# Optimization experiments

Measured on AMD Instinct MI355X. Metric: run time of the kernel, lower is better.

Reference implementation:

```python
import jax, jax.numpy as jnp
import numpy as np

TAU = 2.0      # LIF membrane time constant
VTH = 1.0      # spike threshold
ALPHA = 2.0    # surrogate-gradient sharpness (atan surrogate)
EPS = 1e-5     # BatchNorm eps

@jax.custom_vjp
def spike(u):
    return (u > 0.0).astype(u.dtype)

def _spike_fwd(u):
    return spike(u), u

def _spike_bwd(u, g):
    sg = ALPHA / (2.0 * (1.0 + (jnp.pi / 2.0 * ALPHA * u) ** 2))
    return (g * sg,)

spike.defvjp(_spike_fwd, _spike_bwd)

def lif_time(x):
    # x: [B,T,C,H,W] -> spikes [B,T,C,H,W]; hard-reset LIF, v0 = 0
    xT = jnp.moveaxis(x, 1, 0)  # [T,B,C,H,W]
    def step(v, xt):
        v = v + (xt - v) / TAU
        s = spike(v - VTH)
        return v * (1.0 - s), s
    _, sT = jax.lax.scan(step, jnp.zeros_like(xT[0]), xT)
    return jnp.moveaxis(sT, 0, 1)

def conv2d(x, w, stride, pad):
    return jax.lax.conv_general_dilated(
        x, w, (stride, stride), [(pad, pad), (pad, pad)],
        dimension_numbers=('NCHW', 'OIHW', 'NCHW'))

def bn(x, gamma, beta, mean, var):
    # inference-style BatchNorm2d with running stats; x: [N,C,H,W]
    inv = gamma * jax.lax.rsqrt(var + EPS)
    return x * inv[None, :, None, None] + (beta - mean * inv)[None, :, None, None]

def setup_inputs() -> dict:
    key = jax.random.key(0)
    ks = jax.random.split(key, 16)
    B, T, Cin, Cout, H, W = 16, 8, 128, 256, 56, 56
    d = {}
    d['x_spike'] = (jax.random.uniform(ks[0], (B, T, Cin, H, W)) < 0.2).astype(jnp.float32)
    d['conv1_w'] = jax.random.normal(ks[1], (Cout, Cin, 3, 3), dtype=jnp.float32) * 0.05
    d['conv2_w'] = jax.random.normal(ks[2], (Cout, Cout, 3, 3), dtype=jnp.float32) * 0.05
    d['ds_w'] = jax.random.normal(ks[3], (Cout, Cin, 1, 1), dtype=jnp.float32) * 0.05
    for i, p in enumerate(['n1', 'n2', 'nd']):
        d[p + '_gamma'] = 1.0 + 0.1 * jax.random.normal(ks[4 + i], (Cout,), dtype=jnp.float32)
        d[p + '_beta'] = 0.1 * jax.random.normal(ks[7 + i], (Cout,), dtype=jnp.float32)
        d[p + '_mean'] = 0.01 * jax.random.normal(ks[10 + i], (Cout,), dtype=jnp.float32)
        d[p + '_var'] = jax.random.uniform(ks[13 + i], (Cout,), minval=0.5, maxval=1.5)
    return d

def reference(x_spike, conv1_w, conv2_w, ds_w,
              n1_gamma, n1_beta, n1_mean, n1_var,
              n2_gamma, n2_beta, n2_mean, n2_var,
              nd_gamma, nd_beta, nd_mean, nd_var):
    B, T, Cin, H, W = x_spike.shape
    x_flat = x_spike.reshape(B * T, Cin, H, W)
    # downsample shortcut (1x1 conv stride 2 + BN)
    identity = bn(conv2d(x_flat, ds_w, 2, 0), nd_gamma, nd_beta, nd_mean, nd_var)
    # NOTE: original module runs lif_shortcut on identity but DISCARDS the result
    # (pure state side-effect); it does not affect the output, so it is omitted.
    out = bn(conv2d(x_flat, conv1_w, 2, 1), n1_gamma, n1_beta, n1_mean, n1_var)
    Cout, Ho, Wo = out.shape[1], out.shape[2], out.shape[3]
    out = lif_time(out.reshape(B, T, Cout, Ho, Wo))
    out = bn(conv2d(out.reshape(B * T, Cout, Ho, Wo), conv2_w, 1, 1),
             n2_gamma, n2_beta, n2_mean, n2_var) + identity
    return lif_time(out.reshape(B, T, Cout, Ho, Wo))
```

## Files before the change

### kernel.cpp

```cpp
#include <hip/hip_runtime.h>

#define CIN  128
#define CO   256
#define HIN  56
#define WIN  56
#define P    784
#define HWIN 3136
#define PERT 200704

typedef __attribute__((ext_vector_type(4))) float f32x4;
typedef __attribute__((ext_vector_type(4))) int   i32x4;

__device__ __forceinline__ i32x4 mfma_i8_64(i32x4 a, i32x4 b, i32x4 c) {
    return __builtin_amdgcn_mfma_i32_16x16x64_i8(a, b, c, 0, 0, 0);
}

__device__ __forceinline__ void gld_lds16(const void* g, void* l) {
    __builtin_amdgcn_global_load_lds(
        (const __attribute__((address_space(1))) void*)g,
        (__attribute__((address_space(3))) void*)l, 16, 0, 0);
}

__global__ __launch_bounds__(256) void k_prepA(
    const float* __restrict__ g1, const float* __restrict__ b1,
    const float* __restrict__ m1, const float* __restrict__ v1,
    const float* __restrict__ g2, const float* __restrict__ b2,
    const float* __restrict__ m2, const float* __restrict__ v2,
    const float* __restrict__ gd, const float* __restrict__ bd,
    const float* __restrict__ md, const float* __restrict__ vd,
    const float* __restrict__ w1, const float* __restrict__ w2,
    const float* __restrict__ wd,
    float* __restrict__ bias1, float* __restrict__ bias2,
    float* __restrict__ qscale1, float* __restrict__ scale1,
    float* __restrict__ qscale2, float* __restrict__ scale2)
{
    const int bid = blockIdx.x;
    if (bid == 0) {
        int co = threadIdx.x;
        float inv1 = g1[co] / sqrtf(v1[co] + 1e-5f);
        float inv2 = g2[co] / sqrtf(v2[co] + 1e-5f);
        float invd = gd[co] / sqrtf(vd[co] + 1e-5f);
        bias1[co] = fmaf(-m1[co], inv1, b1[co]);
        bias2[co] = fmaf(-m2[co], inv2, b2[co]) + fmaf(-md[co], invd, bd[co]);
        return;
    }
    const int lane = threadIdx.x & 63;
    if (bid <= 64) {
        int co = (bid - 1) * 4 + (threadIdx.x >> 6);
        float iv = g1[co] / sqrtf(v1[co] + 1e-5f);
        float m = 0.f;
        for (int k = lane; k < 1152; k += 64)
            m = fmaxf(m, fabsf(w1[(size_t)co * 1152 + k] * iv));
#pragma unroll
        for (int off = 32; off > 0; off >>= 1)
            m = fmaxf(m, __shfl_xor(m, off));
        if (lane == 0) {
            int s = (int)floorf(log2f(8355000.0f / m));
            if (s > 44) s = 44;
            qscale1[co] = ldexpf(1.0f, s);
            scale1[co]  = ldexpf(1.0f, -s);
        }
    } else {
        int co = (bid - 65) * 4 + (threadIdx.x >> 6);
        float iv2 = g2[co] / sqrtf(v2[co] + 1e-5f);
        float ivd = gd[co] / sqrtf(vd[co] + 1e-5f);
        float m = 0.f;
        for (int k = lane; k < 2304; k += 64)
            m = fmaxf(m, fabsf(w2[(size_t)co * 2304 + k] * iv2));
        for (int k = lane; k < 128; k += 64)
            m = fmaxf(m, fabsf(wd[(size_t)co * 128 + k] * ivd));
#pragma unroll
        for (int off = 32; off > 0; off >>= 1)
            m = fmaxf(m, __shfl_xor(m, off));
        if (lane == 0) {
            int s = (int)floorf(log2f(8355000.0f / m));
            if (s > 40) s = 40;
            qscale2[co] = ldexpf(1.0f, s);
            scale2[co]  = ldexpf(1.0f, -s);
        }
    }
}

__global__ __launch_bounds__(256) void k_prepB(
    const float* __restrict__ w1, const float* __restrict__ w2,
    const float* __restrict__ wd,
    const float* __restrict__ n1g, const float* __restrict__ n1v,
    const float* __restrict__ n2g, const float* __restrict__ n2v,
    const float* __restrict__ ndg, const float* __restrict__ ndv,
    const float* __restrict__ qscale1, const float* __restrict__ qscale2,
    signed char* __restrict__ pa, signed char* __restrict__ pb,
    signed char* __restrict__ pc,
    signed char* __restrict__ p2a, signed char* __restrict__ p2b,
    signed char* __restrict__ p2c,
    signed char* __restrict__ pda, signed char* __restrict__ pdb,
    signed char* __restrict__ pdc,
    const float* __restrict__ x, unsigned int* __restrict__ xt_p)
{
    const int bid = blockIdx.x;
    if (bid < 72) {
        int i = bid * 256 + threadIdx.x;
        if (i >= 18432) return;
        int tap = i >> 11;
        int r   = i & 2047;
        int kg  = r >> 10;
        int r2  = r & 1023;
        int cf  = r2 >> 6;
        int lane = r2 & 63;
        int co  = cf * 16 + (lane & 15);
        int ci0 = kg * 64 + (lane >> 4) * 16;
        float iv = n1g[co] / sqrtf(n1v[co] + 1e-5f);
        float q  = qscale1[co];
#pragma unroll
        for (int j = 0; j < 16; j++) {
            float w = w1[((size_t)co * CIN + ci0 + j) * 9 + tap] * iv;
            int W = __float2int_rn(w * q);
            int d0 = ((W & 0xFF) ^ 0x80) - 0x80;  W = (W - d0) / 256;
            int d1 = ((W & 0xFF) ^ 0x80) - 0x80;  W = (W - d1) / 256;
            size_t idx = (size_t)i * 16 + j;
            pa[idx] = (signed char)W;
            pb[idx] = (signed char)d1;
            pc[idx] = (signed char)d0;
        }
    } else if (bid < 216) {
        int i = (bid - 72) * 256 + threadIdx.x;
        int tap = i >> 12;
        int r   = i & 4095;
        int kg  = r >> 10;
        int r2  = r & 1023;
        int cf  = r2 >> 6;
        int lane = r2 & 63;
        int co  = cf * 16 + (lane & 15);
        int ci0 = kg * 64 + (lane >> 4) * 16;
        float iv = n2g[co] / sqrtf(n2v[co] + 1e-5f);
        float q  = qscale2[co];
#pragma unroll
        for (int j = 0; j < 16; j++) {
            float w = w2[((size_t)co * CO + ci0 + j) * 9 + tap] * iv;
            int W = __float2int_rn(w * q);
            int d0 = ((W & 0xFF) ^ 0x80) - 0x80;  W = (W - d0) / 256;
            int d1 = ((W & 0xFF) ^ 0x80) - 0x80;  W = (W - d1) / 256;
            size_t idx = (size_t)i * 16 + j;
            p2a[idx] = (signed char)W;
            p2b[idx] = (signed char)d1;
            p2c[idx] = (signed char)d0;
        }
    } else if (bid < 224) {
        int i = (bid - 216) * 256 + threadIdx.x;
        int kg  = i >> 10;
        int r2  = i & 1023;
        int cf  = r2 >> 6;
        int lane = r2 & 63;
        int co  = cf * 16 + (lane & 15);
        int ci0 = kg * 64 + (lane >> 4) * 16;
        float iv = ndg[co] / sqrtf(ndv[co] + 1e-5f);
        float q  = qscale2[co];
#pragma unroll
        for (int j = 0; j < 16; j++) {
            float w = wd[(size_t)co * CIN + ci0 + j] * iv;
            int W = __float2int_rn(w * q);
            int d0 = ((W & 0xFF) ^ 0x80) - 0x80;  W = (W - d0) / 256;
            int d1 = ((W & 0xFF) ^ 0x80) - 0x80;  W = (W - d1) / 256;
            size_t idx = (size_t)i * 16 + j;
            pda[idx] = (signed char)W;
            pdb[idx] = (signed char)d1;
            pdc[idx] = (signed char)d0;
        }
    } else {
        int i = (bid - 224) * 256 + threadIdx.x;
        int pos = i % HWIN;
        int nw  = i / HWIN;
        int w   = nw & 3;
        int n   = nw >> 2;
        const float* xp = x + ((size_t)n * CIN + w * 32) * HWIN + pos;
        unsigned int word = 0;
#pragma unroll
        for (int ci = 0; ci < 32; ci++)
            if (xp[(size_t)ci * HWIN] != 0.f) word |= (1u << ci);
        xt_p[((size_t)n * HWIN + pos) * 4 + w] = word;
    }
}

__global__ __launch_bounds__(256) void k_conv1_mfma(
    const unsigned int* __restrict__ xt_p,
    const signed char* __restrict__ pa,
    const signed char* __restrict__ pb,
    const signed char* __restrict__ pc,
    const float* __restrict__ scale1,
    const float* __restrict__ bias1,
    float* __restrict__ out)
{
    __shared__ unsigned int XWP[2][522 * 2];

    const int n    = blockIdx.x / 7;
    const int rt   = blockIdx.x - n * 7;
    const int r0   = rt * 4;
    const int tid  = threadIdx.x;
    const int wave = tid >> 6;
    const int lane = tid & 63;
    const int l15  = lane & 15;
    const int quad = lane >> 4;
    const int cf   = blockIdx.y * 4 + wave;

    const unsigned int* xp_n = xt_p + (size_t)n * HWIN * 4;
    for (int i = tid; i < 513; i += 256) {
        int row = i / 57, c = i - row * 57;
        int irow = 2 * r0 - 1 + row;
        int iw   = c - 1;
        uint4 val = {0u, 0u, 0u, 0u};
        if (irow >= 0 && iw >= 0)
            val = *(const uint4*)(xp_n + (size_t)(irow * WIN + iw) * 4);
        int base = row * 58 + c;
        XWP[0][base * 2 + 0] = val.x;
        XWP[0][base * 2 + 1] = val.y;
        XWP[1][base * 2 + 0] = val.z;
        XWP[1][base * 2 + 1] = val.w;
    }
    __syncthreads();

    int ib[7];
#pragma unroll
    for (int f = 0; f < 7; f++) {
        int pos = f * 16 + l15;
        int rr = pos / 28, cc = pos - rr * 28;
        ib[f] = (2 * rr) * 58 + 2 * cc;
    }

    const int  qh = quad >> 1;
    const int  ql = (quad & 1) * 16;

    i32x4 accA[7], accB[7], accC[7];
#pragma unroll
    for (int f = 0; f < 7; f++) {
        accA[f] = (i32x4){0, 0, 0, 0};
        accB[f] = (i32x4){0, 0, 0, 0};
        accC[f] = (i32x4){0, 0, 0, 0};
    }

    i32x4 wa, wb, wc, na, nb, nc;
    {
        size_t b0 = (size_t)cf * 1024 + lane * 16;
        wa = *(const i32x4*)(pa + b0);
        wb = *(const i32x4*)(pb + b0);
        wc = *(const i32x4*)(pc + b0);
        na = wa; nb = wb; nc = wc;
    }

    for (int kg = 0; kg < 2; kg++) {
        for (int tap = 0; tap < 9; tap++) {
            int rd = kg * 9 + tap;
            if (rd < 17) {
                int rn = rd + 1, kn = rn / 9, tn = rn - kn * 9;
                size_t b0 = ((size_t)(tn * 2 + kn) * 16 + cf) * 1024 + lane * 16;
                na = *(const i32x4*)(pa + b0);
                nb = *(const i32x4*)(pb + b0);
                nc = *(const i32x4*)(pc + b0);
            }
            const int kh = tap / 3, kw = tap - kh * 3;
            const int tapoff = kh * 58 + kw;
#pragma unroll
            for (int f = 0; f < 7; f++) {
                int base = ib[f] + tapoff;
                uint2 pr = *(const uint2*)&XWP[kg][base * 2];
                unsigned int w32  = qh ? pr.y : pr.x;
                unsigned int bits = (w32 >> ql) & 0xFFFFu;
                uint4 u;
                u.x = ((bits & 15u)         * 0x00204081u) & 0x01010101u;
                u.y = (((bits >> 4) & 15u)  * 0x00204081u) & 0x01010101u;
                u.z = (((bits >> 8) & 15u)  * 0x00204081u) & 0x01010101u;
                u.w = ((bits >> 12)         * 0x00204081u) & 0x01010101u;
                union { uint4 q; i32x4 v; } cv;
                cv.q = u;
                __builtin_amdgcn_s_setprio(1);
                accA[f] = mfma_i8_64(wa, cv.v, accA[f]);
                accB[f] = mfma_i8_64(wb, cv.v, accB[f]);
                accC[f] = mfma_i8_64(wc, cv.v, accC[f]);
                __builtin_amdgcn_s_setprio(0);
            }
            wa = na; wb = nb; wc = nc;
        }
    }

#pragma unroll
    for (int f = 0; f < 7; f++) {
        int pg = rt * 112 + f * 16 + l15;
#pragma unroll
        for (int reg = 0; reg < 4; reg++) {
            int co = cf * 16 + quad * 4 + reg;
            float hi = (float)accA[f][reg];
            float mi = (float)accB[f][reg];
            float lo = (float)accC[f][reg];
            float val = fmaf(hi, 65536.f, fmaf(mi, 256.f, lo));
            out[((size_t)n * CO + co) * P + pg] = fmaf(val, scale1[co], bias1[co]);
        }
    }
}

__global__ __launch_bounds__(256) void k_lif1t(
    const float* __restrict__ pre, unsigned char* __restrict__ st)
{
    __shared__ unsigned short T[16 * 68];
    const int b   = blockIdx.x;
    const int co0 = blockIdx.y * 64;
    const int kg  = blockIdx.y;
    const int p0  = blockIdx.z * 16;
    const int tid  = threadIdx.x;
    const int pcol = tid & 15;
    const int g    = tid >> 4;
    const int pos = p0 + g;
    const int oh  = pos / 28, ow = pos - oh * 28;
    const int f8  = ((((oh + 1) * 30 + ow + 1) >> 1) & 3);
    const int no  = (pcol >> 2) ^ f8;
    const int wb  = (pcol & 3) * 4;
    float v[4] = {0.f, 0.f, 0.f, 0.f};
    for (int t = 0; t < 8; t++) {
        const float* src = pre + (((size_t)(b * 8 + t)) * CO + co0) * P + p0;
        unsigned short s[4];
#pragma unroll
        for (int j = 0; j < 4; j++) {
            int co = g + 16 * j;
            float xv = src[(size_t)co * P + pcol];
            v[j] = v[j] + (xv - v[j]) * 0.5f;
            bool sp = v[j] > 1.0f;
            s[j] = sp ? 1 : 0;
            if (sp) v[j] = 0.f;
        }
        __syncthreads();
#pragma unroll
        for (int j = 0; j < 4; j++) T[pcol * 68 + g + 16 * j] = s[j];
        __syncthreads();
        unsigned char* dst = st + (((size_t)(b * 8 + t) * 4 + kg) * P + pos) * 64
                               + no * 16 + wb;
        uchar4 ov;
        ov.x = (unsigned char)T[g * 68 + pcol * 4 + 0];
        ov.y = (unsigned char)T[g * 68 + pcol * 4 + 1];
        ov.z = (unsigned char)T[g * 68 + pcol * 4 + 2];
        ov.w = (unsigned char)T[g * 68 + pcol * 4 + 3];
        *(uchar4*)dst = ov;
    }
}

__global__ __launch_bounds__(256) void k_conv2_mfma(
    const unsigned char* __restrict__ spike_t,
    const unsigned int* __restrict__ xt_p,
    const signed char* __restrict__ p2a,
    const signed char* __restrict__ p2b,
    const signed char* __restrict__ p2c,
    const signed char* __restrict__ pda,
    const signed char* __restrict__ pdb,
    const signed char* __restrict__ pdc,
    const float* __restrict__ scale2,
    const float* __restrict__ bias2,
    float* __restrict__ out)
{
    __shared__ unsigned char SB[4 * 11520];
    __shared__ unsigned int  XW2[4 * 112];

    const int n    = blockIdx.x / 7;
    const int rt   = blockIdx.x - n * 7;
    const int r0   = rt * 4;
    const int tid  = threadIdx.x;
    const int wave = tid >> 6;
    const int lane = tid & 63;
    const int l15  = lane & 15;
    const int quad = lane >> 4;
    const int cf0  = blockIdx.y * 8 + wave * 2;

    {
        uint4 z = {0u, 0u, 0u, 0u};
        for (int i = tid; i < 2880; i += 256) ((uint4*)SB)[i] = z;
    }
    for (int i = tid; i < 112; i += 256) {
        int r = i / 28, c = i - r * 28;
        uint4 w4 = *(const uint4*)(xt_p + ((size_t)n * HWIN
                    + (2 * (r0 + r)) * WIN + 2 * c) * 4);
        XW2[0 * 112 + i] = w4.x;
        XW2[1 * 112 + i] = w4.y;
        XW2[2 * 112 + i] = w4.z;
        XW2[3 * 112 + i] = w4.w;
    }
    __syncthreads();

    i32x4 dw[2][3][2];
#pragma unroll
    for (int kg = 0; kg < 2; kg++) {
        size_t b0 = ((size_t)kg * 16 + cf0) * 1024 + (size_t)lane * 16;
#pragma unroll
        for (int g = 0; g < 2; g++) {
            dw[kg][0][g] = *(const i32x4*)(pda + b0 + (size_t)g * 1024);
            dw[kg][1][g] = *(const i32x4*)(pdb + b0 + (size_t)g * 1024);
            dw[kg][2][g] = *(const i32x4*)(pdc + b0 + (size_t)g * 1024);
        }
    }

    const char* sp_n = (const char*)spike_t + (size_t)n * 4 * P * 64;
#pragma unroll
    for (int k = 0; k < 3; k++) {
        int idx  = wave * 3 + k;
        int row  = idx >> 1, half = idx & 1;
        int irow = r0 - 1 + row;
        bool ok  = ((unsigned)irow < 28u) && (half == 0 || lane < 48);
        int ldso = row * 1920 + 64 + half * 1024;
        if (ok) {
#pragma unroll
            for (int kg = 0; kg < 4; kg++)
                gld_lds16(sp_n + (size_t)kg * 50176 + (size_t)irow * 1792
                              + half * 1024 + lane * 16,
                          (char*)SB + kg * 11520 + ldso);
        }
    }

    int ib[7];
#pragma unroll
    for (int f = 0; f < 7; f++) {
        int pos = f * 16 + l15;
        int rr = pos / 28, cc = pos - rr * 28;
        ib[f] = rr * 30 + cc;
    }

    i32x4 acc[3][2][7];
#pragma unroll
    for (int p = 0; p < 3; p++)
#pragma unroll
        for (int g = 0; g < 2; g++)
#pragma unroll
            for (int f = 0; f < 7; f++) acc[p][g][f] = (i32x4){0, 0, 0, 0};

#pragma unroll
    for (int kg = 0; kg < 2; kg++) {
        const int wsel = (kg * 2 + (quad >> 1)) * 112;
        const int shv  = (quad & 1) * 16;
#pragma unroll
        for (int f = 0; f < 7; f++) {
            unsigned int w32  = XW2[wsel + f * 16 + l15];
            unsigned int bits = (w32 >> shv) & 0xFFFFu;
            uint4 u;
            u.x = ((bits & 15u)         * 0x00204081u) & 0x01010101u;
            u.y = (((bits >> 4) & 15u)  * 0x00204081u) & 0x01010101u;
            u.z = (((bits >> 8) & 15u)  * 0x00204081u) & 0x01010101u;
            u.w = ((bits >> 12)         * 0x00204081u) & 0x01010101u;
            union { uint4 q; i32x4 v; } cv;
            cv.q = u;
            __builtin_amdgcn_s_setprio(1);
#pragma unroll
            for (int g = 0; g < 2; g++) {
                acc[0][g][f] = mfma_i8_64(dw[kg][0][g], cv.v, acc[0][g][f]);
                acc[1][g][f] = mfma_i8_64(dw[kg][1][g], cv.v, acc[1][g][f]);
                acc[2][g][f] = mfma_i8_64(dw[kg][2][g], cv.v, acc[2][g][f]);
            }
            __builtin_amdgcn_s_setprio(0);
        }
    }
    __syncthreads();

    i32x4 cw[2][3], nx[2][3];
#pragma unroll
    for (int g = 0; g < 2; g++) {
        size_t b0 = ((size_t)(cf0 + g)) * 1024 + (size_t)lane * 16;
        cw[g][0] = *(const i32x4*)(p2a + b0);
        cw[g][1] = *(const i32x4*)(p2b + b0);
        cw[g][2] = *(const i32x4*)(p2c + b0);
        nx[g][0] = cw[g][0]; nx[g][1] = cw[g][1]; nx[g][2] = cw[g][2];
    }

    for (int rd = 0; rd < 36; rd++) {
        if (rd < 35) {
            size_t b0 = ((size_t)(rd + 1) * 16 + cf0) * 1024
                      + (size_t)lane * 16;
#pragma unroll
            for (int g = 0; g < 2; g++) {
                nx[g][0] = *(const i32x4*)(p2a + b0 + (size_t)g * 1024);
                nx[g][1] = *(const i32x4*)(p2b + b0 + (size_t)g * 1024);
                nx[g][2] = *(const i32x4*)(p2c + b0 + (size_t)g * 1024);
            }
        }
        const int tap = rd >> 2, kg = rd & 3;
        const int kh = tap / 3, kw = tap - kh * 3;
        const int tapoff = kh * 30 + kw;
        const int sbase  = kg * 11520;
#pragma unroll
        for (int f = 0; f < 7; f++) {
            int slot = ib[f] + tapoff;
            int sw   = (slot >> 1) & 3;
            i32x4 bfr = *(const i32x4*)(
                SB + sbase + slot * 64 + ((quad ^ sw) * 16));
            __builtin_amdgcn_s_setprio(1);
#pragma unroll
            for (int g = 0; g < 2; g++) {
                acc[0][g][f] = mfma_i8_64(cw[g][0], bfr, acc[0][g][f]);
                acc[1][g][f] = mfma_i8_64(cw[g][1], bfr, acc[1][g][f]);
                acc[2][g][f] = mfma_i8_64(cw[g][2], bfr, acc[2][g][f]);
            }
            __builtin_amdgcn_s_setprio(0);
        }
#pragma unroll
        for (int g = 0; g < 2; g++) {
            cw[g][0] = nx[g][0]; cw[g][1] = nx[g][1]; cw[g][2] = nx[g][2];
        }
    }

#pragma unroll
    for (int g = 0; g < 2; g++)
#pragma unroll
        for (int f = 0; f < 7; f++) {
            int pg = rt * 112 + f * 16 + l15;
#pragma unroll
            for (int reg = 0; reg < 4; reg++) {
                int co = (cf0 + g) * 16 + quad * 4 + reg;
                float A  = (float)acc[0][g][f][reg];
                float Bv = (float)acc[1][g][f][reg];
                float Cv = (float)acc[2][g][f][reg];
                float val = fmaf(A, 65536.f, fmaf(Bv, 256.f, Cv));
                out[((size_t)n * CO + co) * P + pg] = fmaf(val, scale2[co], bias2[co]);
            }
        }
}

__global__ __launch_bounds__(256) void k_lif4(const float4* __restrict__ in,
                                              float4* __restrict__ out)
{
    const int q = PERT / 4;
    const int i = blockIdx.x * 256 + threadIdx.x;
    const int b = i / q;
    const int r = i - b * q;
    const float4* pi = in  + (size_t)(b * 8) * q + r;
    float4*       po = out + (size_t)(b * 8) * q + r;
    float v0 = 0.f, v1 = 0.f, v2 = 0.f, v3 = 0.f;
#pragma unroll
    for (int t = 0; t < 8; t++) {
        float4 xt = pi[(size_t)t * q];
        float4 s;
        v0 = v0 + (xt.x - v0) * 0.5f; s.x = (v0 > 1.0f) ? 1.f : 0.f; if (v0 > 1.0f) v0 = 0.f;
        v1 = v1 + (xt.y - v1) * 0.5f; s.y = (v1 > 1.0f) ? 1.f : 0.f; if (v1 > 1.0f) v1 = 0.f;
        v2 = v2 + (xt.z - v2) * 0.5f; s.z = (v2 > 1.0f) ? 1.f : 0.f; if (v2 > 1.0f) v2 = 0.f;
        v3 = v3 + (xt.w - v3) * 0.5f; s.w = (v3 > 1.0f) ? 1.f : 0.f; if (v3 > 1.0f) v3 = 0.f;
        po[(size_t)t * q] = s;
    }
}

extern "C" void kernel_launch(void* const* d_in, const int* in_sizes, int n_in,
                              void* d_out, int out_size, void* d_ws, size_t ws_size,
                              hipStream_t stream) {
    const float* x   = (const float*)d_in[0];
    const float* w1  = (const float*)d_in[1];
    const float* w2  = (const float*)d_in[2];
    const float* wd  = (const float*)d_in[3];
    const float* n1g = (const float*)d_in[4];
    const float* n1b = (const float*)d_in[5];
    const float* n1m = (const float*)d_in[6];
    const float* n1v = (const float*)d_in[7];
    const float* n2g = (const float*)d_in[8];
    const float* n2b = (const float*)d_in[9];
    const float* n2m = (const float*)d_in[10];
    const float* n2v = (const float*)d_in[11];
    const float* ndg = (const float*)d_in[12];
    const float* ndb = (const float*)d_in[13];
    const float* ndm = (const float*)d_in[14];
    const float* ndv = (const float*)d_in[15];

    float* out = (float*)d_out;

    char* w = (char*)d_ws;
    unsigned char*  spike_t = (unsigned char*)w;
    signed char*    p2a     = (signed char*)(w + 25690112);
    signed char*    p2b     = (signed char*)(w + 26279936);
    signed char*    p2c     = (signed char*)(w + 26869760);
    signed char*    pa      = (signed char*)(w + 27459584);
    signed char*    pb      = (signed char*)(w + 27754496);
    signed char*    pc      = (signed char*)(w + 28049408);
    signed char*    pda     = (signed char*)(w + 28344320);
    signed char*    pdb     = (signed char*)(w + 28377088);
    signed char*    pdc     = (signed char*)(w + 28409856);
    float*          qscale1 = (float*)(w + 28442624);
    float*          scale1f = (float*)(w + 28443648);
    float*          qscale2 = (float*)(w + 28444672);
    float*          scale2f = (float*)(w + 28445696);
    float*          bias2   = (float*)(w + 28446720);
    float*          bias1   = (float*)(w + 28447744);
    unsigned int*   xt_p    = (unsigned int*)(w + 28451840);

    k_prepA<<<129, 256, 0, stream>>>(
        n1g, n1b, n1m, n1v, n2g, n2b, n2m, n2v, ndg, ndb, ndm, ndv,
        w1, w2, wd, bias1, bias2, qscale1, scale1f, qscale2, scale2f);
    k_prepB<<<224 + (128 * 4 * HWIN) / 256, 256, 0, stream>>>(
        w1, w2, wd, n1g, n1v, n2g, n2v, ndg, ndv, qscale1, qscale2,
        pa, pb, pc, p2a, p2b, p2c, pda, pdb, pdc, x, xt_p);

    k_conv1_mfma<<<dim3(896, 4), 256, 0, stream>>>(
        xt_p, pa, pb, pc, scale1f, bias1, out);
    k_lif1t<<<dim3(16, 4, 49), 256, 0, stream>>>(out, spike_t);
    k_conv2_mfma<<<dim3(896, 2), 256, 0, stream>>>(
        spike_t, xt_p, p2a, p2b, p2c, pda, pdb, pdc, scale2f, bias2, out);
    k_lif4<<<(16 * (PERT / 4)) / 256, 256, 0, stream>>>(
        (const float4*)out, (float4*)out);
}
```

Before: 710.3 us.

## Fuse conv1 with first LIF over time; double-buffer conv2 spike tiles

Conv1 now loops over all 8 timesteps inside one block, keeping the LIF membrane state in registers and writing packed spike bytes directly. This removes the fp32 pre-activation round trip through global memory and the separate LIF kernel. Conv2 shrinks its shared spike buffer to two channel groups and streams the four groups with double-buffered async loads, which should raise occupancy. In exchange conv1 runs far fewer blocks (896 of 128 threads instead of 3584 of 256) and serializes the timesteps, so it has less parallelism and reloads weights every step.

Measured after the change: 808.7 us. 13.8% more time.

```diff
diff --git a/kernel.cpp b/kernel.cpp
--- a/kernel.cpp
+++ b/kernel.cpp
@@ -180,162 +180,151 @@
     }
 }
 
-__global__ __launch_bounds__(256) void k_conv1_mfma(
+__global__ __launch_bounds__(128) void k_conv1_lif(
     const unsigned int* __restrict__ xt_p,
     const signed char* __restrict__ pa,
     const signed char* __restrict__ pb,
     const signed char* __restrict__ pc,
     const float* __restrict__ scale1,
     const float* __restrict__ bias1,
-    float* __restrict__ out)
+    unsigned char* __restrict__ st)
 {
     __shared__ unsigned int XWP[2][522 * 2];
 
-    const int n    = blockIdx.x / 7;
-    const int rt   = blockIdx.x - n * 7;
+    const int b    = blockIdx.x / 7;
+    const int rt   = blockIdx.x - b * 7;
     const int r0   = rt * 4;
     const int tid  = threadIdx.x;
     const int wave = tid >> 6;
     const int lane = tid & 63;
     const int l15  = lane & 15;
     const int quad = lane >> 4;
-    const int cf   = blockIdx.y * 4 + wave;
-
-    const unsigned int* xp_n = xt_p + (size_t)n * HWIN * 4;
-    for (int i = tid; i < 513; i += 256) {
-        int row = i / 57, c = i - row * 57;
-        int irow = 2 * r0 - 1 + row;
-        int iw   = c - 1;
-        uint4 val = {0u, 0u, 0u, 0u};
-        if (irow >= 0 && iw >= 0)
-            val = *(const uint4*)(xp_n + (size_t)(irow * WIN + iw) * 4);
-        int base = row * 58 + c;
-        XWP[0][base * 2 + 0] = val.x;
-        XWP[0][base * 2 + 1] = val.y;
-        XWP[1][base * 2 + 0] = val.z;
-        XWP[1][base * 2 + 1] = val.w;
-    }
-    __syncthreads();
-
-    int ib[7];
+    const int cf   = blockIdx.y * 2 + wave;
+    const int kg_o = cf >> 2;
+    const int sub  = cf & 3;
+
+    int ib[7], f8v[7], posg[7];
 #pragma unroll
     for (int f = 0; f < 7; f++) {
         int pos = f * 16 + l15;
         int rr = pos / 28, cc = pos - rr * 28;
         ib[f] = (2 * rr) * 58 + 2 * cc;
-    }
-
-    const int  qh = quad >> 1;
-    const int  ql = (quad & 1) * 16;
-
-    i32x4 accA[7], accB[7], accC[7];
-#pragma unroll
-    for (int f = 0; f < 7; f++) {
-        accA[f] = (i32x4){0, 0, 0, 0};
-        accB[f] = (i32x4){0, 0, 0, 0};
-        accC[f] = (i32x4){0, 0, 0, 0};
-    }
-
-    i32x4 wa, wb, wc, na, nb, nc;
-    {
-        size_t b0 = (size_t)cf * 1024 + lane * 16;
-        wa = *(const i32x4*)(pa + b0);
-        wb = *(const i32x4*)(pb + b0);
-        wc = *(const i32x4*)(pc + b0);
-        na = wa; nb = wb; nc = wc;
-    }
-
-    for (int kg = 0; kg < 2; kg++) {
-        for (int tap = 0; tap < 9; tap++) {
-            int rd = kg * 9 + tap;
-            if (rd < 17) {
-                int rn = rd + 1, kn = rn / 9, tn = rn - kn * 9;
-                size_t b0 = ((size_t)(tn * 2 + kn) * 16 + cf) * 1024 + lane * 16;
-                na = *(const i32x4*)(pa + b0);
-                nb = *(const i32x4*)(pb + b0);
-                nc = *(const i32x4*)(pc + b0);
-            }
-            const int kh = tap / 3, kw = tap - kh * 3;
-            const int tapoff = kh * 58 + kw;
-#pragma unroll
-            for (int f = 0; f < 7; f++) {
-                int base = ib[f] + tapoff;
-                uint2 pr = *(const uint2*)&XWP[kg][base * 2];
-                unsigned int w32  = qh ? pr.y : pr.x;
-                unsigned int bits = (w32 >> ql) & 0xFFFFu;
-                uint4 u;
-                u.x = ((bits & 15u)         * 0x00204081u) & 0x01010101u;
-                u.y = (((bits >> 4) & 15u)  * 0x00204081u) & 0x01010101u;
-                u.z = (((bits >> 8) & 15u)  * 0x00204081u) & 0x01010101u;
-                u.w = ((bits >> 12)         * 0x00204081u) & 0x01010101u;
-                union { uint4 q; i32x4 v; } cv;
-                cv.q = u;
-                __builtin_amdgcn_s_setprio(1);
-                accA[f] = mfma_i8_64(wa, cv.v, accA[f]);
-                accB[f] = mfma_i8_64(wb, cv.v, accB[f]);
-                accC[f] = mfma_i8_64(wc, cv.v, accC[f]);
-                __builtin_amdgcn_s_setprio(0);
-            }
-            wa = na; wb = nb; wc = nc;
-        }
-    }
-
-#pragma unroll
-    for (int f = 0; f < 7; f++) {
-        int pg = rt * 112 + f * 16 + l15;
-#pragma unroll
-        for (int reg = 0; reg < 4; reg++) {
-            int co = cf * 16 + quad * 4 + reg;
-            float hi = (float)accA[f][reg];
-            float mi = (float)accB[f][reg];
-            float lo = (float)accC[f][reg];
-            float val = fmaf(hi, 65536.f, fmaf(mi, 256.f, lo));
-            out[((size_t)n * CO + co) * P + pg] = fmaf(val, scale1[co], bias1[co]);
-        }
-    }
-}
-
-__global__ __launch_bounds__(256) void k_lif1t(
-    const float* __restrict__ pre, unsigned char* __restrict__ st)
-{
-    __shared__ unsigned short T[16 * 68];
-    const int b   = blockIdx.x;
-    const int co0 = blockIdx.y * 64;
-    const int kg  = blockIdx.y;
-    const int p0  = blockIdx.z * 16;
-    const int tid  = threadIdx.x;
-    const int pcol = tid & 15;
-    const int g    = tid >> 4;
-    const int pos = p0 + g;
-    const int oh  = pos / 28, ow = pos - oh * 28;
-    const int f8  = ((((oh + 1) * 30 + ow + 1) >> 1) & 3);
-    const int no  = (pcol >> 2) ^ f8;
-    const int wb  = (pcol & 3) * 4;
-    float v[4] = {0.f, 0.f, 0.f, 0.f};
+        int pg = rt * 112 + pos;
+        posg[f] = pg;
+        int oh = pg / 28, ow = pg - oh * 28;
+        f8v[f] = ((((oh + 1) * 30 + ow + 1) >> 1) & 3);
+    }
+
+    const int qh = quad >> 1;
+    const int ql = (quad & 1) * 16;
+
+    float s1[4], b1[4];
+#pragma unroll
+    for (int reg = 0; reg < 4; reg++) {
+        int co = cf * 16 + quad * 4 + reg;
+        s1[reg] = scale1[co];
+        b1[reg] = bias1[co];
+    }
+
+    float v[7][4];
+#pragma unroll
+    for (int f = 0; f < 7; f++)
+#pragma unroll
+        for (int r = 0; r < 4; r++) v[f][r] = 0.f;
+
     for (int t = 0; t < 8; t++) {
-        const float* src = pre + (((size_t)(b * 8 + t)) * CO + co0) * P + p0;
-        unsigned short s[4];
-#pragma unroll
-        for (int j = 0; j < 4; j++) {
-            int co = g + 16 * j;
-            float xv = src[(size_t)co * P + pcol];
-            v[j] = v[j] + (xv - v[j]) * 0.5f;
-            bool sp = v[j] > 1.0f;
-            s[j] = sp ? 1 : 0;
-            if (sp) v[j] = 0.f;
-        }
+        const int n = b * 8 + t;
         __syncthreads();
-#pragma unroll
-        for (int j = 0; j < 4; j++) T[pcol * 68 + g + 16 * j] = s[j];
+        const unsigned int* xp_n = xt_p + (size_t)n * HWIN * 4;
+        for (int i = tid; i < 513; i += 128) {
+            int row = i / 57, c = i - row * 57;
+            int irow = 2 * r0 - 1 + row;
+            int iw   = c - 1;
+            uint4 val = {0u, 0u, 0u, 0u};
+            if (irow >= 0 && iw >= 0)
+                val = *(const uint4*)(xp_n + (size_t)(irow * WIN + iw) * 4);
+            int base = row * 58 + c;
+            XWP[0][base * 2 + 0] = val.x;
+            XWP[0][base * 2 + 1] = val.y;
+            XWP[1][base * 2 + 0] = val.z;
+            XWP[1][base * 2 + 1] = val.w;
+        }
         __syncthreads();
-        unsigned char* dst = st + (((size_t)(b * 8 + t) * 4 + kg) * P + pos) * 64
-                               + no * 16 + wb;
-        uchar4 ov;
-        ov.x = (unsigned char)T[g * 68 + pcol * 4 + 0];
-        ov.y = (unsigned char)T[g * 68 + pcol * 4 + 1];
-        ov.z = (unsigned char)T[g * 68 + pcol * 4 + 2];
-        ov.w = (unsigned char)T[g * 68 + pcol * 4 + 3];
-        *(uchar4*)dst = ov;
+
+        i32x4 accA[7], accB[7], accC[7];
+#pragma unroll
+        for (int f = 0; f < 7; f++) {
+            accA[f] = (i32x4){0, 0, 0, 0};
+            accB[f] = (i32x4){0, 0, 0, 0};
+            accC[f] = (i32x4){0, 0, 0, 0};
+        }
+
+        i32x4 wa, wb, wc, na, nb, nc;
+        {
+            size_t b0 = (size_t)cf * 1024 + lane * 16;
+            wa = *(const i32x4*)(pa + b0);
+            wb = *(const i32x4*)(pb + b0);
+            wc = *(const i32x4*)(pc + b0);
+            na = wa; nb = wb; nc = wc;
+        }
+
+        for (int kg = 0; kg < 2; kg++) {
+            for (int tap = 0; tap < 9; tap++) {
+                int rd = kg * 9 + tap;
+                {
+                    int rn = (rd == 17) ? 0 : rd + 1;
+                    int kn = rn / 9, tn = rn - kn * 9;
+                    size_t b0 = ((size_t)(tn * 2 + kn) * 16 + cf) * 1024
+                              + lane * 16;
+                    na = *(const i32x4*)(pa + b0);
+                    nb = *(const i32x4*)(pb + b0);
+                    nc = *(const i32x4*)(pc + b0);
+                }
+                const int kh = tap / 3, kw = tap - kh * 3;
+                const int tapoff = kh * 58 + kw;
+#pragma unroll
+                for (int f = 0; f < 7; f++) {
+                    int base = ib[f] + tapoff;
+                    uint2 pr = *(const uint2*)&XWP[kg][base * 2];
+                    unsigned int w32  = qh ? pr.y : pr.x;
+                    unsigned int bits = (w32 >> ql) & 0xFFFFu;
+                    uint4 u;
+                    u.x = ((bits & 15u)         * 0x00204081u) & 0x01010101u;
+                    u.y = (((bits >> 4) & 15u)  * 0x00204081u) & 0x01010101u;
+                    u.z = (((bits >> 8) & 15u)  * 0x00204081u) & 0x01010101u;
+                    u.w = ((bits >> 12)         * 0x00204081u) & 0x01010101u;
+                    union { uint4 q; i32x4 v; } cv;
+                    cv.q = u;
+                    __builtin_amdgcn_s_setprio(1);
+                    accA[f] = mfma_i8_64(wa, cv.v, accA[f]);
+                    accB[f] = mfma_i8_64(wb, cv.v, accB[f]);
+                    accC[f] = mfma_i8_64(wc, cv.v, accC[f]);
+                    __builtin_amdgcn_s_setprio(0);
+                }
+                wa = na; wb = nb; wc = nc;
+            }
+        }
+
+#pragma unroll
+        for (int f = 0; f < 7; f++) {
+            unsigned int pack = 0u;
+#pragma unroll
+            for (int reg = 0; reg < 4; reg++) {
+                float hi = (float)accA[f][reg];
+                float mi = (float)accB[f][reg];
+                float lo = (float)accC[f][reg];
+                float val = fmaf(hi, 65536.f, fmaf(mi, 256.f, lo));
+                float xv  = fmaf(val, s1[reg], b1[reg]);
+                float vn  = v[f][reg] + (xv - v[f][reg]) * 0.5f;
+                bool  sp  = vn > 1.0f;
+                v[f][reg] = sp ? 0.f : vn;
+                if (sp) pack |= (1u << (reg * 8));
+            }
+            unsigned char* dst = st
+                + (((size_t)(n * 4 + kg_o)) * P + posg[f]) * 64
+                + (sub ^ f8v[f]) * 16 + quad * 4;
+            *(unsigned int*)dst = pack;
+        }
     }
 }
 
@@ -352,7 +341,7 @@
     const float* __restrict__ bias2,
     float* __restrict__ out)
 {
-    __shared__ unsigned char SB[4 * 11520];
+    __shared__ unsigned char SB[2 * 11520];
     __shared__ unsigned int  XW2[4 * 112];
 
     const int n    = blockIdx.x / 7;
@@ -367,7 +356,7 @@
 
     {
         uint4 z = {0u, 0u, 0u, 0u};
-        for (int i = tid; i < 2880; i += 256) ((uint4*)SB)[i] = z;
+        for (int i = tid; i < 1440; i += 256) ((uint4*)SB)[i] = z;
     }
     for (int i = tid; i < 112; i += 256) {
         int r = i / 28, c = i - r * 28;
@@ -380,34 +369,26 @@
     }
     __syncthreads();
 
-    i32x4 dw[2][3][2];
-#pragma unroll
-    for (int kg = 0; kg < 2; kg++) {
-        size_t b0 = ((size_t)kg * 16 + cf0) * 1024 + (size_t)lane * 16;
-#pragma unroll
-        for (int g = 0; g < 2; g++) {
-            dw[kg][0][g] = *(const i32x4*)(pda + b0 + (size_t)g * 1024);
-            dw[kg][1][g] = *(const i32x4*)(pdb + b0 + (size_t)g * 1024);
-            dw[kg][2][g] = *(const i32x4*)(pdc + b0 + (size_t)g * 1024);
-        }
-    }
-
-    const char* sp_n = (const char*)spike_t + (size_t)n * 4 * P * 64;
+    int  g_irow[3], g_lds[3];
+    bool g_ok[3];
+    int  g_half[3];
 #pragma unroll
     for (int k = 0; k < 3; k++) {
         int idx  = wave * 3 + k;
         int row  = idx >> 1, half = idx & 1;
         int irow = r0 - 1 + row;
-        bool ok  = ((unsigned)irow < 28u) && (half == 0 || lane < 48);
-        int ldso = row * 1920 + 64 + half * 1024;
-        if (ok) {
-#pragma unroll
-            for (int kg = 0; kg < 4; kg++)
-                gld_lds16(sp_n + (size_t)kg * 50176 + (size_t)irow * 1792
-                              + half * 1024 + lane * 16,
-                          (char*)SB + kg * 11520 + ldso);
-        }
-    }
+        g_irow[k] = irow;
+        g_half[k] = half;
+        g_ok[k]   = ((unsigned)irow < 28u) && (half == 0 || lane < 48);
+        g_lds[k]  = row * 1920 + 64 + half * 1024;
+    }
+    const char* sp_n = (const char*)spike_t + (size_t)n * 4 * P * 64;
+
+#pragma unroll
+    for (int k = 0; k < 3; k++)
+        if (g_ok[k])
+            gld_lds16(sp_n + (size_t)g_irow[k] * 1792 + g_half[k] * 1024 + lane * 16,
+                      (char*)SB + g_lds[k]);
 
     int ib[7];
 #pragma unroll
@@ -425,8 +406,15 @@
 #pragma unroll
             for (int f = 0; f < 7; f++) acc[p][g][f] = (i32x4){0, 0, 0, 0};
 
-#pragma unroll
     for (int kg = 0; kg < 2; kg++) {
+        size_t b0 = ((size_t)kg * 16 + cf0) * 1024 + (size_t)lane * 16;
+        i32x4 d0[2], d1[2], d2[2];
+#pragma unroll
+        for (int g = 0; g < 2; g++) {
+            d0[g] = *(const i32x4*)(pda + b0 + (size_t)g * 1024);
+            d1[g] = *(const i32x4*)(pdb + b0 + (size_t)g * 1024);
+            d2[g] = *(const i32x4*)(pdc + b0 + (size_t)g * 1024);
+        }
         const int wsel = (kg * 2 + (quad >> 1)) * 112;
         const int shv  = (quad & 1) * 16;
 #pragma unroll
@@ -440,14 +428,12 @@
             u.w = ((bits >> 12)         * 0x00204081u) & 0x01010101u;
             union { uint4 q; i32x4 v; } cv;
             cv.q = u;
-            __builtin_amdgcn_s_setprio(1);
 #pragma unroll
             for (int g = 0; g < 2; g++) {
-                acc[0][g][f] = mfma_i8_64(dw[kg][0][g], cv.v, acc[0][g][f]);
-                acc[1][g][f] = mfma_i8_64(dw[kg][1][g], cv.v, acc[1][g][f]);
-                acc[2][g][f] = mfma_i8_64(dw[kg][2][g], cv.v, acc[2][g][f]);
-            }
-            __builtin_amdgcn_s_setprio(0);
+                acc[0][g][f] = mfma_i8_64(d0[g], cv.v, acc[0][g][f]);
+                acc[1][g][f] = mfma_i8_64(d1[g], cv.v, acc[1][g][f]);
+                acc[2][g][f] = mfma_i8_64(d2[g], cv.v, acc[2][g][f]);
+            }
         }
     }
     __syncthreads();
@@ -462,40 +448,51 @@
         nx[g][0] = cw[g][0]; nx[g][1] = cw[g][1]; nx[g][2] = cw[g][2];
     }
 
-    for (int rd = 0; rd < 36; rd++) {
-        if (rd < 35) {
-            size_t b0 = ((size_t)(rd + 1) * 16 + cf0) * 1024
-                      + (size_t)lane * 16;
+    for (int c = 0; c < 4; c++) {
+        if (c < 3) {
+            const char* base = sp_n + (size_t)(c + 1) * 50176;
+            char* dstb = (char*)SB + ((c + 1) & 1) * 11520;
+#pragma unroll
+            for (int k = 0; k < 3; k++)
+                if (g_ok[k])
+                    gld_lds16(base + (size_t)g_irow[k] * 1792 + g_half[k] * 1024 + lane * 16,
+                              dstb + g_lds[k]);
+        }
+        const int bufsh = (c & 1) * 11520;
+        for (int tap = 0; tap < 9; tap++) {
+            int rd = c * 9 + tap;
+            if (rd < 35) {
+                int rn = rd + 1, cn = rn / 9, tn = rn - cn * 9;
+                size_t b0 = ((size_t)(tn * 4 + cn) * 16 + cf0) * 1024
+                          + (size_t)lane * 16;
+#pragma unroll
+                for (int g = 0; g < 2; g++) {
+                    nx[g][0] = *(const i32x4*)(p2a + b0 + (size_t)g * 1024);
+                    nx[g][1] = *(const i32x4*)(p2b + b0 + (size_t)g * 1024);
+                    nx[g][2] = *(const i32x4*)(p2c + b0 + (size_t)g * 1024);
+                }
+            }
+            const int kh = tap / 3, kw = tap - kh * 3;
+            const int tapoff = kh * 30 + kw;
+#pragma unroll
+            for (int f = 0; f < 7; f++) {
+                int slot = ib[f] + tapoff;
+                int sw   = (slot >> 1) & 3;
+                i32x4 bfr = *(const i32x4*)(
+                    SB + bufsh + slot * 64 + ((quad ^ sw) * 16));
+#pragma unroll
+                for (int g = 0; g < 2; g++) {
+                    acc[0][g][f] = mfma_i8_64(cw[g][0], bfr, acc[0][g][f]);
+                    acc[1][g][f] = mfma_i8_64(cw[g][1], bfr, acc[1][g][f]);
+                    acc[2][g][f] = mfma_i8_64(cw[g][2], bfr, acc[2][g][f]);
+                }
+            }
 #pragma unroll
             for (int g = 0; g < 2; g++) {
-                nx[g][0] = *(const i32x4*)(p2a + b0 + (size_t)g * 1024);
-                nx[g][1] = *(const i32x4*)(p2b + b0 + (size_t)g * 1024);
-                nx[g][2] = *(const i32x4*)(p2c + b0 + (size_t)g * 1024);
-            }
-        }
-        const int tap = rd >> 2, kg = rd & 3;
-        const int kh = tap / 3, kw = tap - kh * 3;
-        const int tapoff = kh * 30 + kw;
-        const int sbase  = kg * 11520;
-#pragma unroll
-        for (int f = 0; f < 7; f++) {
-            int slot = ib[f] + tapoff;
-            int sw   = (slot >> 1) & 3;
-            i32x4 bfr = *(const i32x4*)(
-                SB + sbase + slot * 64 + ((quad ^ sw) * 16));
-            __builtin_amdgcn_s_setprio(1);
-#pragma unroll
-            for (int g = 0; g < 2; g++) {
-                acc[0][g][f] = mfma_i8_64(cw[g][0], bfr, acc[0][g][f]);
-                acc[1][g][f] = mfma_i8_64(cw[g][1], bfr, acc[1][g][f]);
-                acc[2][g][f] = mfma_i8_64(cw[g][2], bfr, acc[2][g][f]);
-            }
-            __builtin_amdgcn_s_setprio(0);
-        }
-#pragma unroll
-        for (int g = 0; g < 2; g++) {
-            cw[g][0] = nx[g][0]; cw[g][1] = nx[g][1]; cw[g][2] = nx[g][2];
-        }
+                cw[g][0] = nx[g][0]; cw[g][1] = nx[g][1]; cw[g][2] = nx[g][2];
+            }
+        }
+        __syncthreads();
     }
 
 #pragma unroll
@@ -585,9 +582,8 @@
         w1, w2, wd, n1g, n1v, n2g, n2v, ndg, ndv, qscale1, qscale2,
         pa, pb, pc, p2a, p2b, p2c, pda, pdb, pdc, x, xt_p);
 
-    k_conv1_mfma<<<dim3(896, 4), 256, 0, stream>>>(
-        xt_p, pa, pb, pc, scale1f, bias1, out);
-    k_lif1t<<<dim3(16, 4, 49), 256, 0, stream>>>(out, spike_t);
+    k_conv1_lif<<<dim3(112, 8), 128, 0, stream>>>(
+        xt_p, pa, pb, pc, scale1f, bias1, spike_t);
     k_conv2_mfma<<<dim3(896, 2), 256, 0, stream>>>(
         spike_t, xt_p, p2a, p2b, p2c, pda, pdb, pdc, scale2f, bias2, out);
     k_lif4<<<(16 * (PERT / 4)) / 256, 256, 0, stream>>>(
```

## Double-buffer conv2 spike tiles in LDS per channel group

Applied to the files above, without the earlier changes.

The conv2 kernel no longer stages all four 64-channel spike groups in LDS up front. It keeps two buffers and prefetches the next group with async global-to-LDS loads while the current group is consumed, reordering the reduction loop to channel-group-outer, tap-inner with matching weight indexing. This halves LDS per block, which may allow more resident blocks and overlaps the spike loads with MFMA work. It also loads the downsample weights per iteration instead of holding them all in registers, and drops the s_setprio hints. The cost is an extra barrier per channel group, and accumulator register pressure may still cap occupancy.

New measurement: 709.2 us. About the same (-0.2%).

```diff
diff --git a/kernel.cpp b/kernel.cpp
--- a/kernel.cpp
+++ b/kernel.cpp
@@ -352,7 +352,7 @@
     const float* __restrict__ bias2,
     float* __restrict__ out)
 {
-    __shared__ unsigned char SB[4 * 11520];
+    __shared__ unsigned char SB[2 * 11520];
     __shared__ unsigned int  XW2[4 * 112];
 
     const int n    = blockIdx.x / 7;
@@ -367,7 +367,7 @@
 
     {
         uint4 z = {0u, 0u, 0u, 0u};
-        for (int i = tid; i < 2880; i += 256) ((uint4*)SB)[i] = z;
+        for (int i = tid; i < 1440; i += 256) ((uint4*)SB)[i] = z;
     }
     for (int i = tid; i < 112; i += 256) {
         int r = i / 28, c = i - r * 28;
@@ -380,34 +380,26 @@
     }
     __syncthreads();
 
-    i32x4 dw[2][3][2];
-#pragma unroll
-    for (int kg = 0; kg < 2; kg++) {
-        size_t b0 = ((size_t)kg * 16 + cf0) * 1024 + (size_t)lane * 16;
-#pragma unroll
-        for (int g = 0; g < 2; g++) {
-            dw[kg][0][g] = *(const i32x4*)(pda + b0 + (size_t)g * 1024);
-            dw[kg][1][g] = *(const i32x4*)(pdb + b0 + (size_t)g * 1024);
-            dw[kg][2][g] = *(const i32x4*)(pdc + b0 + (size_t)g * 1024);
-        }
-    }
-
-    const char* sp_n = (const char*)spike_t + (size_t)n * 4 * P * 64;
+    int  g_irow[3], g_lds[3];
+    bool g_ok[3];
+    int  g_half[3];
 #pragma unroll
     for (int k = 0; k < 3; k++) {
         int idx  = wave * 3 + k;
         int row  = idx >> 1, half = idx & 1;
         int irow = r0 - 1 + row;
-        bool ok  = ((unsigned)irow < 28u) && (half == 0 || lane < 48);
-        int ldso = row * 1920 + 64 + half * 1024;
-        if (ok) {
-#pragma unroll
-            for (int kg = 0; kg < 4; kg++)
-                gld_lds16(sp_n + (size_t)kg * 50176 + (size_t)irow * 1792
-                              + half * 1024 + lane * 16,
-                          (char*)SB + kg * 11520 + ldso);
-        }
-    }
+        g_irow[k] = irow;
+        g_half[k] = half;
+        g_ok[k]   = ((unsigned)irow < 28u) && (half == 0 || lane < 48);
+        g_lds[k]  = row * 1920 + 64 + half * 1024;
+    }
+    const char* sp_n = (const char*)spike_t + (size_t)n * 4 * P * 64;
+
+#pragma unroll
+    for (int k = 0; k < 3; k++)
+        if (g_ok[k])
+            gld_lds16(sp_n + (size_t)g_irow[k] * 1792 + g_half[k] * 1024 + lane * 16,
+                      (char*)SB + g_lds[k]);
 
     int ib[7];
 #pragma unroll
@@ -425,8 +417,15 @@
 #pragma unroll
             for (int f = 0; f < 7; f++) acc[p][g][f] = (i32x4){0, 0, 0, 0};
 
-#pragma unroll
     for (int kg = 0; kg < 2; kg++) {
+        size_t b0 = ((size_t)kg * 16 + cf0) * 1024 + (size_t)lane * 16;
+        i32x4 d0[2], d1[2], d2[2];
+#pragma unroll
+        for (int g = 0; g < 2; g++) {
+            d0[g] = *(const i32x4*)(pda + b0 + (size_t)g * 1024);
+            d1[g] = *(const i32x4*)(pdb + b0 + (size_t)g * 1024);
+            d2[g] = *(const i32x4*)(pdc + b0 + (size_t)g * 1024);
+        }
         const int wsel = (kg * 2 + (quad >> 1)) * 112;
         const int shv  = (quad & 1) * 16;
 #pragma unroll
@@ -440,14 +439,12 @@
             u.w = ((bits >> 12)         * 0x00204081u) & 0x01010101u;
             union { uint4 q; i32x4 v; } cv;
             cv.q = u;
-            __builtin_amdgcn_s_setprio(1);
 #pragma unroll
             for (int g = 0; g < 2; g++) {
-                acc[0][g][f] = mfma_i8_64(dw[kg][0][g], cv.v, acc[0][g][f]);
-                acc[1][g][f] = mfma_i8_64(dw[kg][1][g], cv.v, acc[1][g][f]);
-                acc[2][g][f] = mfma_i8_64(dw[kg][2][g], cv.v, acc[2][g][f]);
+                acc[0][g][f] = mfma_i8_64(d0[g], cv.v, acc[0][g][f]);
+                acc[1][g][f] = mfma_i8_64(d1[g], cv.v, acc[1][g][f]);
+                acc[2][g][f] = mfma_i8_64(d2[g], cv.v, acc[2][g][f]);
             }
-            __builtin_amdgcn_s_setprio(0);
         }
     }
     __syncthreads();
@@ -462,40 +459,51 @@
         nx[g][0] = cw[g][0]; nx[g][1] = cw[g][1]; nx[g][2] = cw[g][2];
     }
 
-    for (int rd = 0; rd < 36; rd++) {
-        if (rd < 35) {
-            size_t b0 = ((size_t)(rd + 1) * 16 + cf0) * 1024
-                      + (size_t)lane * 16;
+    for (int c = 0; c < 4; c++) {
+        if (c < 3) {
+            const char* base = sp_n + (size_t)(c + 1) * 50176;
+            char* dstb = (char*)SB + ((c + 1) & 1) * 11520;
+#pragma unroll
+            for (int k = 0; k < 3; k++)
+                if (g_ok[k])
+                    gld_lds16(base + (size_t)g_irow[k] * 1792 + g_half[k] * 1024 + lane * 16,
+                              dstb + g_lds[k]);
+        }
+        const int bufsh = (c & 1) * 11520;
+        for (int tap = 0; tap < 9; tap++) {
+            int rd = c * 9 + tap;
+            if (rd < 35) {
+                int rn = rd + 1, cn = rn / 9, tn = rn - cn * 9;
+                size_t b0 = ((size_t)(tn * 4 + cn) * 16 + cf0) * 1024
+                          + (size_t)lane * 16;
+#pragma unroll
+                for (int g = 0; g < 2; g++) {
+                    nx[g][0] = *(const i32x4*)(p2a + b0 + (size_t)g * 1024);
+                    nx[g][1] = *(const i32x4*)(p2b + b0 + (size_t)g * 1024);
+                    nx[g][2] = *(const i32x4*)(p2c + b0 + (size_t)g * 1024);
+                }
+            }
+            const int kh = tap / 3, kw = tap - kh * 3;
+            const int tapoff = kh * 30 + kw;
+#pragma unroll
+            for (int f = 0; f < 7; f++) {
+                int slot = ib[f] + tapoff;
+                int sw   = (slot >> 1) & 3;
+                i32x4 bfr = *(const i32x4*)(
+                    SB + bufsh + slot * 64 + ((quad ^ sw) * 16));
+#pragma unroll
+                for (int g = 0; g < 2; g++) {
+                    acc[0][g][f] = mfma_i8_64(cw[g][0], bfr, acc[0][g][f]);
+                    acc[1][g][f] = mfma_i8_64(cw[g][1], bfr, acc[1][g][f]);
+                    acc[2][g][f] = mfma_i8_64(cw[g][2], bfr, acc[2][g][f]);
+                }
+            }
 #pragma unroll
             for (int g = 0; g < 2; g++) {
-                nx[g][0] = *(const i32x4*)(p2a + b0 + (size_t)g * 1024);
-                nx[g][1] = *(const i32x4*)(p2b + b0 + (size_t)g * 1024);
-                nx[g][2] = *(const i32x4*)(p2c + b0 + (size_t)g * 1024);
+                cw[g][0] = nx[g][0]; cw[g][1] = nx[g][1]; cw[g][2] = nx[g][2];
             }
         }
-        const int tap = rd >> 2, kg = rd & 3;
-        const int kh = tap / 3, kw = tap - kh * 3;
-        const int tapoff = kh * 30 + kw;
-        const int sbase  = kg * 11520;
-#pragma unroll
-        for (int f = 0; f < 7; f++) {
-            int slot = ib[f] + tapoff;
-            int sw   = (slot >> 1) & 3;
-            i32x4 bfr = *(const i32x4*)(
-                SB + sbase + slot * 64 + ((quad ^ sw) * 16));
-            __builtin_amdgcn_s_setprio(1);
-#pragma unroll
-            for (int g = 0; g < 2; g++) {
-                acc[0][g][f] = mfma_i8_64(cw[g][0], bfr, acc[0][g][f]);
-                acc[1][g][f] = mfma_i8_64(cw[g][1], bfr, acc[1][g][f]);
-                acc[2][g][f] = mfma_i8_64(cw[g][2], bfr, acc[2][g][f]);
-            }
-            __builtin_amdgcn_s_setprio(0);
-        }
-#pragma unroll
-        for (int g = 0; g < 2; g++) {
-            cw[g][0] = nx[g][0]; cw[g][1] = nx[g][1]; cw[g][2] = nx[g][2];
-        }
+        __syncthreads();
     }
 
 #pragma unroll
```
